# Kernel optimization log

Hardware: AMD Instinct MI355X
Metric: run time of the kernel (lower is better)

Reference implementation:

```python
import jax, jax.numpy as jnp
import numpy as np

D_MODEL = 2048
N_HEADS = 16
HEAD_DIM = D_MODEL // N_HEADS  # 128
MAX_T = 2048
ROPE_BASE = 10000.0


def _rope_tables(head_dim, max_t, base):
    inv = 1.0 / (base ** (np.arange(0, head_dim, 2, dtype=np.float32) / head_dim))
    t = np.arange(max_t, dtype=np.float32)
    fr = np.outer(t, inv)  # (T, head_dim//2)
    return jnp.asarray(np.cos(fr)), jnp.asarray(np.sin(fr))


def setup_inputs() -> dict:
    key = jax.random.key(0)
    k1, k2, k3 = jax.random.split(key, 3)
    B, T = 2, 2048
    x = jax.random.normal(k1, (B, T, D_MODEL), dtype=jnp.float32)
    Wqkv = jax.random.normal(k2, (3 * D_MODEL, D_MODEL), dtype=jnp.float32) * 0.02
    Wout = jax.random.normal(k3, (D_MODEL, D_MODEL), dtype=jnp.float32) * 0.02
    cos, sin = _rope_tables(HEAD_DIM, MAX_T, ROPE_BASE)
    rope_mask = jnp.arange(N_HEADS) < (N_HEADS // 2)  # first 8 heads RoPE, rest NoPE
    return {"x": x, "Wqkv": Wqkv, "Wout": Wout, "cos": cos, "sin": sin, "rope_mask": rope_mask}


def _apply_rope(t, cos, sin):
    # t: (B,H,T,hd); pairs are consecutive elements (x0,x1),(x2,x3),...
    B, H, T, hd = t.shape
    tr = t.reshape(B, H, T, hd // 2, 2)
    c = cos[:T][None, None, :, :]
    s = sin[:T][None, None, :, :]
    re = tr[..., 0] * c - tr[..., 1] * s
    im = tr[..., 0] * s + tr[..., 1] * c
    return jnp.stack([re, im], axis=-1).reshape(B, H, T, hd)


def reference(x, Wqkv, Wout, cos, sin, rope_mask):
    B, T, D = x.shape
    H = rope_mask.shape[0]
    hd = D // H
    qkv = x @ Wqkv.T  # (B,T,3D)
    q, k, v = jnp.split(qkv, 3, axis=-1)
    def heads(a):
        return a.reshape(B, T, H, hd).transpose(0, 2, 1, 3)  # (B,H,T,hd)
    q, k, v = heads(q), heads(k), heads(v)
    m = rope_mask[None, :, None, None]  # broadcast over (B,H,T,hd)
    q = jnp.where(m, _apply_rope(q, cos, sin), q)
    k = jnp.where(m, _apply_rope(k, cos, sin), k)
    scale = 1.0 / jnp.sqrt(jnp.asarray(hd, dtype=q.dtype))
    scores = jnp.einsum('bhtd,bhsd->bhts', q, k) * scale
    causal = jnp.tril(jnp.ones((T, T), dtype=bool))
    scores = jnp.where(causal[None, None], scores, jnp.asarray(-jnp.inf, dtype=scores.dtype))
    p = jax.nn.softmax(scores, axis=-1)
    out = jnp.einsum('bhts,bhsd->bhtd', p, v)
    out = out.transpose(0, 2, 1, 3).reshape(B, T, D)
    return out @ Wout.T
```

## Files before the change

### kernel.cpp

```cpp
#include <hip/hip_runtime.h>
#include <stdint.h>

typedef unsigned short u16;
typedef __attribute__((ext_vector_type(8))) short short8;
typedef __attribute__((ext_vector_type(4))) short s16x4;
typedef __attribute__((ext_vector_type(4))) float f32x4;
typedef __attribute__((ext_vector_type(16))) float f32x16;

__device__ __forceinline__ u16 f2bf(float f) {
  uint32_t x = __float_as_uint(f);
  x += 0x7fff + ((x >> 16) & 1);
  return (u16)(x >> 16);
}
__device__ __forceinline__ float bf2f(u16 u) {
  return __uint_as_float(((uint32_t)u) << 16);
}
__device__ __forceinline__ f32x4 mfma16(short8 a, short8 b, f32x4 c) {
  return __builtin_amdgcn_mfma_f32_16x16x32_bf16(a, b, c, 0, 0, 0);
}
__device__ __forceinline__ f32x16 mfma32(short8 a, short8 b, f32x16 c) {
  return __builtin_amdgcn_mfma_f32_32x32x16_bf16(a, b, c, 0, 0, 0);
}
__device__ __forceinline__ f32x4 mfma16k16(s16x4 a, s16x4 b, f32x4 c) {
  return __builtin_amdgcn_mfma_f32_16x16x16bf16_1k(a, b, c, 0, 0, 0);
}
__device__ __forceinline__ void gld16(const u16* g, u16* l) {
  __builtin_amdgcn_global_load_lds(
      (const __attribute__((address_space(1))) unsigned int*)g,
      (__attribute__((address_space(3))) unsigned int*)l, 16, 0, 0);
}
__device__ __forceinline__ float exp2a(float x) {
  float r;
  asm("v_exp_f32 %0, %1" : "=v"(r) : "v"(x));
  return r;
}

__global__ __launch_bounds__(256) void cvt_all(const float* __restrict__ x,
                                               const float* __restrict__ wqkv,
                                               const float* __restrict__ wout,
                                               u16* __restrict__ xb,
                                               u16* __restrict__ wqkvb,
                                               u16* __restrict__ woutb) {
  long i = ((long)blockIdx.x * 256 + threadIdx.x) * 8;
  const float* s;
  u16* d;
  long off;
  if (i < 8388608) {
    s = x; d = xb; off = i;
  } else if (i < 20971520) {
    s = wqkv; d = wqkvb; off = i - 8388608;
  } else {
    s = wout; d = woutb; off = i - 20971520;
  }
  f32x4 a = *(const f32x4*)(s + off);
  f32x4 b = *(const f32x4*)(s + off + 4);
  short8 o;
#pragma unroll
  for (int j = 0; j < 4; j++) {
    o[j] = (short)f2bf(a[j]);
    o[j + 4] = (short)f2bf(b[j]);
  }
  *(short8*)(d + off) = o;
}

template <int EPI>
__global__ __launch_bounds__(256) void gemm_bt(const u16* __restrict__ A,
                                               const u16* __restrict__ B,
                                               int K, void* __restrict__ Cv, int N) {
  __shared__ __align__(16) u16 SMEM[8448];
  u16* As = SMEM;
  u16* Bs = SMEM + 4096;
  const int m0 = blockIdx.y * 128, n0 = blockIdx.x * 128;
  const int t = threadIdx.x, w = t >> 6, lane = t & 63;
  const int l31 = lane & 31, half = lane >> 5;
  const int rb = (w >> 1) * 64, cb = (w & 1) * 64;
  f32x16 acc[2][2] = {};
  const int rowS = w * 16 + (lane >> 2);
  const int cS = ((lane & 3) - (rowS >> 1)) & 3;
  const u16* ag = A + (size_t)(m0 + rowS) * K + cS * 8;
  const u16* bg = B + (size_t)(n0 + rowS) * K + cS * 8;
  u16* al = As + w * 512 + lane * 8;
  u16* bl = Bs + w * 512 + lane * 8;
  const size_t rowskip = (size_t)64 * K;
  const int p0 = ((0 * 2 + half + (l31 >> 1)) & 3) * 8;
  const int p1 = ((1 * 2 + half + (l31 >> 1)) & 3) * 8;
  for (int k0 = 0; k0 < K; k0 += 32) {
    __syncthreads();
    gld16(ag, al);
    gld16(ag + rowskip, al + 2048);
    gld16(bg, bl);
    gld16(bg + rowskip, bl + 2048);
    ag += 32;
    bg += 32;
    __syncthreads();
    short8 af[2][2], bfr[2][2];
#pragma unroll
    for (int mi = 0; mi < 2; mi++) {
      af[mi][0] = *(const short8*)&As[(rb + mi * 32 + l31) * 32 + p0];
      af[mi][1] = *(const short8*)&As[(rb + mi * 32 + l31) * 32 + p1];
    }
#pragma unroll
    for (int ni = 0; ni < 2; ni++) {
      bfr[ni][0] = *(const short8*)&Bs[(cb + ni * 32 + l31) * 32 + p0];
      bfr[ni][1] = *(const short8*)&Bs[(cb + ni * 32 + l31) * 32 + p1];
    }
#pragma unroll
    for (int kh = 0; kh < 2; kh++)
#pragma unroll
      for (int mi = 0; mi < 2; mi++)
#pragma unroll
        for (int ni = 0; ni < 2; ni++)
          acc[mi][ni] = mfma32(af[mi][kh], bfr[ni][kh], acc[mi][ni]);
  }

  if (EPI == 0) {
    const int which = n0 >> 11;
    const int hh = (n0 & 2047) >> 7;
    const int bb = m0 >> 11, tt0 = m0 & 2047;
    u16* q3 = (u16*)Cv;
    if (which == 2) {
      u16* vbase = q3 + 16777216 + ((size_t)(bb * 16 + hh) * 128) * 2048;
#pragma unroll
      for (int mi = 0; mi < 2; mi++)
#pragma unroll
        for (int ni = 0; ni < 2; ni++) {
          int di = cb + ni * 32 + l31;
          int trow = tt0 + rb + mi * 32 + half * 4;
#pragma unroll
          for (int rg2 = 0; rg2 < 4; rg2++) {
            s16x4 st;
#pragma unroll
            for (int j = 0; j < 4; j++) st[j] = (short)f2bf(acc[mi][ni][rg2 * 4 + j]);
            *(s16x4*)(vbase + (size_t)di * 2048 + trow + rg2 * 8) = st;
          }
        }
    } else {
      const float sc = (which == 0) ? 0.1275174f : 1.0f;
      u16* base = q3 + (size_t)which * 8388608 + ((size_t)(bb * 16 + hh) * 2048) * 128;
#pragma unroll
      for (int mi = 0; mi < 2; mi++)
#pragma unroll
        for (int ni = 0; ni < 2; ni++) {
          int di = cb + ni * 32 + l31;
          int trow = tt0 + rb + mi * 32 + half * 4;
#pragma unroll
          for (int reg = 0; reg < 16; reg++) {
            int tt = trow + (reg & 3) + 8 * (reg >> 2);
            base[(size_t)tt * 128 + di] = f2bf(acc[mi][ni][reg] * sc);
          }
        }
    }
  } else {
    float* Es = (float*)SMEM;
    float* C = (float*)Cv;
#pragma unroll
    for (int r = 0; r < 4; r++) {
      __syncthreads();
      if ((w >> 1) == (r >> 1)) {
        const int mi = r & 1;
#pragma unroll
        for (int ni = 0; ni < 2; ni++) {
          int col = cb + ni * 32 + l31;
#pragma unroll
          for (int reg = 0; reg < 16; reg++) {
            int lrow = (reg & 3) + 8 * (reg >> 2) + half * 4;
            Es[lrow * 132 + col] = acc[mi][ni][reg];
          }
        }
      }
      __syncthreads();
#pragma unroll
      for (int it = 0; it < 4; it++) {
        int idx = it * 256 + t;
        int row = idx >> 5, ch = idx & 31;
        f32x4 vv = *(const f32x4*)&Es[row * 132 + ch * 4];
        *(f32x4*)&C[(size_t)(m0 + r * 32 + row) * N + n0 + ch * 4] = vv;
      }
    }
  }
}

__global__ __launch_bounds__(256) void rope_k(u16* __restrict__ q, u16* __restrict__ k,
                                              const float* __restrict__ cosT,
                                              const float* __restrict__ sinT) {
  int t = threadIdx.x;
  int row = blockIdx.x * 4 + (t >> 6);
  int i = t & 63;
  int b = row >> 14;
  int h = (row >> 11) & 7;
  int tp = row & 2047;
  size_t base = ((size_t)((b * 16 + h) * 2048 + tp)) * 128 + 2 * i;
  float c = cosT[tp * 64 + i], s = sinT[tp * 64 + i];
  {
    uint32_t u = *(uint32_t*)(q + base);
    float x0 = bf2f((u16)(u & 0xffff)), x1 = bf2f((u16)(u >> 16));
    float re = x0 * c - x1 * s, im = x0 * s + x1 * c;
    *(uint32_t*)(q + base) = (uint32_t)f2bf(re) | ((uint32_t)f2bf(im) << 16);
  }
  {
    uint32_t u = *(uint32_t*)(k + base);
    float x0 = bf2f((u16)(u & 0xffff)), x1 = bf2f((u16)(u >> 16));
    float re = x0 * c - x1 * s, im = x0 * s + x1 * c;
    *(uint32_t*)(k + base) = (uint32_t)f2bf(re) | ((uint32_t)f2bf(im) << 16);
  }
}

__global__ __launch_bounds__(256, 2) void attn_k(const u16* __restrict__ qh,
                                                 const u16* __restrict__ kh,
                                                 const u16* __restrict__ vTh,
                                                 u16* __restrict__ attno) {
  __shared__ __align__(16) u16 Ks[8192];
  __shared__ __align__(16) u16 Vt[8192];
  const int i = blockIdx.x;
  const int jj = i & 255, half = i >> 8;
  const int bh = jj >> 3, t8 = jj & 7;
  const int qt = half ? (15 - t8) : t8;
  const int q0 = qt * 128;
  const int t = threadIdx.x, w = t >> 6, lane = t & 63;
  const int quad = lane >> 4, l15 = lane & 15;
  const size_t bhoff = (size_t)bh * 262144;

  short8 qb[2][4];
  {
    const u16* qp = qh + bhoff + (size_t)(q0 + w * 32 + l15) * 128 + quad * 8;
#pragma unroll
    for (int qq = 0; qq < 2; qq++)
#pragma unroll
      for (int ks = 0; ks < 4; ks++)
        qb[qq][ks] = *(const short8*)(qp + qq * 2048 + ks * 32);
  }
  f32x4 of[2][8] = {};
  float mst[2] = {-1e30f, -1e30f}, lst[2] = {0.f, 0.f};
  const int nkt = 2 * qt + 2;
  const int wq0 = q0 + w * 32;

  for (int kt = 0; kt < nkt; kt++) {
    const int k0 = kt * 64;
    __syncthreads();
    {
#pragma unroll
      for (int it = 0; it < 4; it++) {
        int L = it * 256 + t;
        int key = L >> 4, c = L & 15;
        gld16(kh + bhoff + (size_t)(k0 + key) * 128 + ((c ^ (key & 15)) * 8),
              Ks + (size_t)L * 8);
      }
#pragma unroll
      for (int it = 0; it < 4; it++) {
        int L = it * 256 + t;
        int d = L >> 3, c = L & 7;
        gld16(vTh + bhoff + (size_t)d * 2048 + k0 + ((c ^ (d & 7)) * 8),
              Vt + (size_t)L * 8);
      }
    }
    __syncthreads();
    if (k0 <= wq0 + 31) {
      f32x4 sacc[2][4];
#pragma unroll
      for (int qq = 0; qq < 2; qq++)
#pragma unroll
        for (int kk = 0; kk < 4; kk++) sacc[qq][kk] = (f32x4){0.f, 0.f, 0.f, 0.f};
#pragma unroll
      for (int kk = 0; kk < 4; kk++) {
        short8 kf[4];
#pragma unroll
        for (int ks = 0; ks < 4; ks++)
          kf[ks] = *(const short8*)&Ks[(kk * 16 + l15) * 128 + ((ks * 4 + quad) ^ l15) * 8];
#pragma unroll
        for (int qq = 0; qq < 2; qq++)
#pragma unroll
          for (int ks = 0; ks < 4; ks++)
            sacc[qq][kk] = mfma16(kf[ks], qb[qq][ks], sacc[qq][kk]);
      }
      const bool needmask = (k0 + 63 > wq0);
      s16x4 pf[2][4];
      float alpha[2];
#pragma unroll
      for (int qq = 0; qq < 2; qq++) {
        const int qg = wq0 + qq * 16 + l15;
        if (needmask) {
#pragma unroll
          for (int kk = 0; kk < 4; kk++)
#pragma unroll
            for (int rg = 0; rg < 4; rg++)
              if (k0 + kk * 16 + quad * 4 + rg > qg) sacc[qq][kk][rg] = -1e30f;
        }
        float pm = -1e30f;
#pragma unroll
        for (int kk = 0; kk < 4; kk++)
#pragma unroll
          for (int rg = 0; rg < 4; rg++) pm = fmaxf(pm, sacc[qq][kk][rg]);
        pm = fmaxf(pm, __shfl_xor(pm, 16));
        pm = fmaxf(pm, __shfl_xor(pm, 32));
        float mnew = fmaxf(mst[qq], pm);
        alpha[qq] = exp2a(mst[qq] - mnew);
        mst[qq] = mnew;
        float ps = 0.f;
#pragma unroll
        for (int kk = 0; kk < 4; kk++) {
          float e0 = exp2a(sacc[qq][kk][0] - mnew);
          float e1 = exp2a(sacc[qq][kk][1] - mnew);
          float e2 = exp2a(sacc[qq][kk][2] - mnew);
          float e3 = exp2a(sacc[qq][kk][3] - mnew);
          ps += (e0 + e1) + (e2 + e3);
          pf[qq][kk][0] = (short)f2bf(e0);
          pf[qq][kk][1] = (short)f2bf(e1);
          pf[qq][kk][2] = (short)f2bf(e2);
          pf[qq][kk][3] = (short)f2bf(e3);
        }
        ps += __shfl_xor(ps, 16);
        ps += __shfl_xor(ps, 32);
        lst[qq] = lst[qq] * alpha[qq] + ps;
      }
#pragma unroll
      for (int qq = 0; qq < 2; qq++) {
        if (!__all(alpha[qq] == 1.0f)) {
          float a = alpha[qq];
#pragma unroll
          for (int df = 0; df < 8; df++) of[qq][df] *= a;
        }
      }
#pragma unroll
      for (int df = 0; df < 8; df++) {
        s16x4 vf[4];
#pragma unroll
        for (int kk = 0; kk < 4; kk++)
          vf[kk] = *(const s16x4*)&Vt[(df * 16 + l15) * 64 +
                                      ((kk * 2 + (quad >> 1)) ^ (l15 & 7)) * 8 +
                                      (quad & 1) * 4];
#pragma unroll
        for (int qq = 0; qq < 2; qq++)
#pragma unroll
          for (int kk = 0; kk < 4; kk++)
            of[qq][df] = mfma16k16(vf[kk], pf[qq][kk], of[qq][df]);
      }
    }
  }
  const int b = bh >> 4, h = bh & 15;
#pragma unroll
  for (int qq = 0; qq < 2; qq++) {
    float linv = 1.0f / lst[qq];
    const size_t row = (size_t)(b * 2048 + q0 + w * 32 + qq * 16 + l15);
#pragma unroll
    for (int df = 0; df < 8; df++) {
      s16x4 o;
#pragma unroll
      for (int rg = 0; rg < 4; rg++) o[rg] = (short)f2bf(of[qq][df][rg] * linv);
      *(s16x4*)(attno + row * 2048 + h * 128 + df * 16 + quad * 4) = o;
    }
  }
}

extern "C" void kernel_launch(void* const* d_in, const int* in_sizes, int n_in,
                              void* d_out, int out_size, void* d_ws, size_t ws_size,
                              hipStream_t stream) {
  const float* x = (const float*)d_in[0];
  const float* Wqkv = (const float*)d_in[1];
  const float* Wout = (const float*)d_in[2];
  const float* cosT = (const float*)d_in[3];
  const float* sinT = (const float*)d_in[4];
  float* out = (float*)d_out;
  char* ws = (char*)d_ws;
  u16* qkvh = (u16*)(ws + 0);
  u16* woutb = (u16*)(ws + 50331648);
  u16* xb = (u16*)(ws + 58720256);
  u16* wqkvb = (u16*)(ws + 75497472);
  u16* attno = wqkvb;

  cvt_all<<<12288, 256, 0, stream>>>(x, Wqkv, Wout, xb, wqkvb, woutb);
  gemm_bt<0><<<dim3(48, 32), 256, 0, stream>>>(xb, wqkvb, 2048, (void*)qkvh, 0);
  rope_k<<<8192, 256, 0, stream>>>(qkvh, qkvh + 8388608, cosT, sinT);
  attn_k<<<512, 256, 0, stream>>>(qkvh, qkvh + 8388608, qkvh + 16777216, attno);
  gemm_bt<1><<<dim3(16, 32), 256, 0, stream>>>(attno, woutb, 2048, (void*)out, 2048);
}
```

Measured before the change: 414.5 us.

## Add 256x256-tile pipelined QKV GEMM with 4-stage LDS ring and block swizzle

Replaces the 128x128 QKV projection GEMM with a dedicated 512-thread kernel using 256x256 tiles, a 4-deep global_load_lds prefetch ring with explicit vmcnt waits, split A/B staging interleaved with MFMA halves, setprio around the MFMA bursts, and a grouped block-index swizzle for L2 reuse. The epilogue writes Q (prescaled), K and transposed V directly in head layout. This is meant to raise arithmetic intensity and overlap loads with compute. The cost is much higher LDS use (128KB per block) and register pressure, and Q/K stores are scattered 2-byte writes.

```diff
diff --git a/kernel.cpp b/kernel.cpp
--- a/kernel.cpp
+++ b/kernel.cpp
@@ -34,6 +34,8 @@
   asm("v_exp_f32 %0, %1" : "=v"(r) : "v"(x));
   return r;
 }
+
+#define WAIT_VM(n) asm volatile("s_waitcnt vmcnt(" #n ")" ::: "memory")
 
 __global__ __launch_bounds__(256) void cvt_all(const float* __restrict__ x,
                                                const float* __restrict__ wqkv,
@@ -61,6 +63,129 @@
     o[j + 4] = (short)f2bf(b[j]);
   }
   *(short8*)(d + off) = o;
+}
+
+__global__ __launch_bounds__(512, 2) void gemm_qkv(const u16* __restrict__ A,
+                                                   const u16* __restrict__ Bw,
+                                                   u16* __restrict__ q3) {
+  __shared__ __align__(16) u16 SA[32768];
+  __shared__ __align__(16) u16 SB[32768];
+  const int id = blockIdx.x;
+  const int swz = (id & 7) * 48 + (id >> 3);
+  const int by = swz & 15, bx = swz >> 4;
+  const int m0 = by * 256, n0 = bx * 256;
+  const int t = threadIdx.x, w = t >> 6, lane = t & 63;
+  const int quad = lane >> 4, l15 = lane & 15;
+  const int wm = w >> 2, wn = w & 3;
+  const int rS = t >> 2, pS = t & 3;
+  const int cS = (pS - (rS >> 1)) & 3;
+  const size_t arow = (size_t)(m0 + rS) * 2048 + cS * 8;
+  const size_t brow = (size_t)(n0 + rS) * 2048 + cS * 8;
+
+#define STAGE_A(kt)                                      \
+  {                                                      \
+    const u16* ga_ = A + arow + (size_t)(kt) * 32;       \
+    u16* la_ = SA + ((kt) & 3) * 8192 + t * 8;           \
+    gld16(ga_, la_);                                     \
+    gld16(ga_ + (size_t)128 * 2048, la_ + 4096);         \
+  }
+#define STAGE_B(kt)                                      \
+  {                                                      \
+    const u16* gb_ = Bw + brow + (size_t)(kt) * 32;      \
+    u16* lb_ = SB + ((kt) & 3) * 8192 + t * 8;           \
+    gld16(gb_, lb_);                                     \
+    gld16(gb_ + (size_t)128 * 2048, lb_ + 4096);         \
+  }
+
+  f32x4 acc[8][4] = {};
+  const int pq = ((quad + (l15 >> 1)) & 3) * 8;
+
+  STAGE_A(0); STAGE_B(0);
+  STAGE_A(1); STAGE_B(1);
+  STAGE_A(2); STAGE_B(2);
+  WAIT_VM(8);
+  __builtin_amdgcn_s_barrier();
+
+#pragma unroll 1
+  for (int tau = 0; tau < 64; ++tau) {
+    const u16* Sa = SA + (tau & 3) * 8192;
+    const u16* Sb = SB + (tau & 3) * 8192;
+    short8 af[4], bfr[4];
+#pragma unroll
+    for (int i = 0; i < 4; i++)
+      af[i] = *(const short8*)&Sa[(wm * 128 + i * 16 + l15) * 32 + pq];
+#pragma unroll
+    for (int n = 0; n < 4; n++)
+      bfr[n] = *(const short8*)&Sb[(wn * 64 + n * 16 + l15) * 32 + pq];
+    if (tau < 61) STAGE_A(tau + 3);
+    __builtin_amdgcn_s_barrier();
+    __builtin_amdgcn_s_setprio(1);
+#pragma unroll
+    for (int mi = 0; mi < 4; mi++)
+#pragma unroll
+      for (int ni = 0; ni < 4; ni++)
+        acc[mi][ni] = mfma16(af[mi], bfr[ni], acc[mi][ni]);
+    __builtin_amdgcn_s_setprio(0);
+    __builtin_amdgcn_s_barrier();
+#pragma unroll
+    for (int i = 0; i < 4; i++)
+      af[i] = *(const short8*)&Sa[(wm * 128 + 64 + i * 16 + l15) * 32 + pq];
+    if (tau < 61) STAGE_B(tau + 3);
+    __builtin_amdgcn_s_barrier();
+    __builtin_amdgcn_s_setprio(1);
+#pragma unroll
+    for (int mi = 0; mi < 4; mi++)
+#pragma unroll
+      for (int ni = 0; ni < 4; ni++)
+        acc[4 + mi][ni] = mfma16(af[mi], bfr[ni], acc[4 + mi][ni]);
+    __builtin_amdgcn_s_setprio(0);
+    if (tau < 61) {
+      WAIT_VM(8);
+    } else if (tau == 61) {
+      WAIT_VM(4);
+    } else if (tau == 62) {
+      WAIT_VM(0);
+    }
+    __builtin_amdgcn_s_barrier();
+  }
+#undef STAGE_A
+#undef STAGE_B
+
+  const int which = n0 >> 11;
+  const int bb = m0 >> 11, tt0 = m0 & 2047;
+  if (which == 2) {
+    u16* vbase = q3 + 16777216;
+#pragma unroll
+    for (int ni = 0; ni < 4; ni++) {
+      const int gcol = (n0 & 2047) + wn * 64 + ni * 16 + l15;
+      const int hh = gcol >> 7, di = gcol & 127;
+      u16* vb = vbase + ((size_t)(bb * 16 + hh) * 128 + di) * 2048;
+#pragma unroll
+      for (int mi = 0; mi < 8; mi++) {
+        const int tloc = tt0 + wm * 128 + mi * 16 + quad * 4;
+        s16x4 st;
+#pragma unroll
+        for (int r = 0; r < 4; r++) st[r] = (short)f2bf(acc[mi][ni][r]);
+        *(s16x4*)(vb + tloc) = st;
+      }
+    }
+  } else {
+    const float sc = (which == 0) ? 0.1275174f : 1.0f;
+    u16* base = q3 + (size_t)which * 8388608;
+#pragma unroll
+    for (int ni = 0; ni < 4; ni++) {
+      const int gcol = (n0 & 2047) + wn * 64 + ni * 16 + l15;
+      const int hh = gcol >> 7, di = gcol & 127;
+      u16* qb = base + ((size_t)(bb * 16 + hh) * 2048) * 128 + di;
+#pragma unroll
+      for (int mi = 0; mi < 8; mi++) {
+        const int tloc = tt0 + wm * 128 + mi * 16 + quad * 4;
+#pragma unroll
+        for (int r = 0; r < 4; r++)
+          qb[(size_t)(tloc + r) * 128] = f2bf(acc[mi][ni][r] * sc);
+      }
+    }
+  }
 }
 
 template <int EPI>
@@ -368,7 +493,7 @@
   u16* attno = wqkvb;
 
   cvt_all<<<12288, 256, 0, stream>>>(x, Wqkv, Wout, xb, wqkvb, woutb);
-  gemm_bt<0><<<dim3(48, 32), 256, 0, stream>>>(xb, wqkvb, 2048, (void*)qkvh, 0);
+  gemm_qkv<<<384, 512, 0, stream>>>(xb, wqkvb, qkvh);
   rope_k<<<8192, 256, 0, stream>>>(qkvh, qkvh + 8388608, cosT, sinT);
   attn_k<<<512, 256, 0, stream>>>(qkvh, qkvh + 8388608, qkvh + 16777216, attno);
   gemm_bt<1><<<dim3(16, 32), 256, 0, stream>>>(attno, woutb, 2048, (void*)out, 2048);
```

Measured after the change: 408.2 us. No clear change (-1.5%).
